# Kernel tuning notes

Measured on AMD Instinct MI355X. Metric: run time of the kernel, lower is better.

The kernel has to match this reference:

```python
import jax, jax.numpy as jnp
import numpy as np

DIM, HEADS, DIM_HEAD = 1024, 16, 64


def setup_inputs() -> dict:
    key = jax.random.key(0)
    k1, k2, k3, k4 = jax.random.split(key, 4)
    x = jax.random.normal(k1, (4, 2048, DIM), dtype=jnp.float32)
    # nn.Linear(dim, 3*dim, bias=False): weight [3*dim, dim]; y = x @ W.T
    W_qkv = jax.random.normal(k2, (3 * DIM, DIM), dtype=jnp.float32) * (DIM ** -0.5)
    W_proj = jax.random.normal(k3, (DIM, DIM), dtype=jnp.float32) * (DIM ** -0.5)
    b_proj = jax.random.normal(k4, (DIM,), dtype=jnp.float32) * 0.02
    return {"x": x, "W_qkv": W_qkv, "W_proj": W_proj, "b_proj": b_proj}


def reference(x, W_qkv, W_proj, b_proj):
    B, N, C = x.shape
    H, D = HEADS, DIM_HEAD
    scale = D ** -0.5
    qkv = x @ W_qkv.T                                   # [B, N, 3C]
    qkv = qkv.reshape(B, N, 3, H, D).transpose(2, 0, 3, 1, 4)  # [3, B, H, N, D]
    q, k, v = qkv[0], qkv[1], qkv[2]
    dots = jnp.einsum('bhid,bhjd->bhij', q, k) * scale  # [B, H, N, N]
    attn = jax.nn.softmax(dots, axis=-1)
    out = jnp.einsum('bhij,bhjd->bhid', attn, v)        # [B, H, N, D]
    out = out.transpose(0, 2, 1, 3).reshape(B, N, C)
    return out @ W_proj.T + b_proj
```

## Files before the change

### kernel.cpp

```cpp
#include <hip/hip_runtime.h>
#include <hip/hip_bf16.h>
#include <stdint.h>

typedef __bf16 bf16x4 __attribute__((ext_vector_type(4)));
typedef __bf16 bf16x8 __attribute__((ext_vector_type(8)));
typedef float  f32x4  __attribute__((ext_vector_type(4)));

#define LOG2E 1.44269504088896f

__device__ __forceinline__ bf16x8 cat8(bf16x4 a, bf16x4 b) {
    bf16x8 r;
    for (int i = 0; i < 4; ++i) { r[i] = a[i]; r[i + 4] = b[i]; }
    return r;
}

__device__ __forceinline__ void gl2lds16(const __bf16* g, __bf16* l) {
    __builtin_amdgcn_global_load_lds(
        (const __attribute__((address_space(1))) void*)g,
        (__attribute__((address_space(3))) void*)l, 16, 0, 0);
}

__global__ __launch_bounds__(256) void cvt_f32_bf16(const float* __restrict__ in,
                                                    __bf16* __restrict__ out) {
    size_t i = ((size_t)blockIdx.x * 256 + threadIdx.x) * 8;
    float4 a = ((const float4*)(in + i))[0];
    float4 b = ((const float4*)(in + i))[1];
    bf16x8 v;
    v[0] = (__bf16)a.x; v[1] = (__bf16)a.y; v[2] = (__bf16)a.z; v[3] = (__bf16)a.w;
    v[4] = (__bf16)b.x; v[5] = (__bf16)b.y; v[6] = (__bf16)b.z; v[7] = (__bf16)b.w;
    *(bf16x8*)(out + i) = v;
}

template<typename TC>
__global__ __launch_bounds__(256) void gemm_bt_bf16(
    const __bf16* __restrict__ A, const __bf16* __restrict__ B,
    const float* __restrict__ bias, TC* __restrict__ C,
    int M, int N, int K, int lda, int ldb, int ldc)
{
    __shared__ __bf16 As[128][32];
    __shared__ __bf16 Bs[128][32];
    const int tid = threadIdx.x;
    const int wave = tid >> 6, lane = tid & 63;
    const int lr = lane & 15, lq = lane >> 4;
    const int m0 = blockIdx.y * 128, n0 = blockIdx.x * 128;
    const int wm = (wave >> 1) * 64, wn = (wave & 1) * 64;

    f32x4 acc[4][4] = {};

    const int sr = lane >> 2;
    const int sc = (lane & 3) * 8;
    const __bf16* ag[2]; const __bf16* bg[2];
    __bf16* alds[2]; __bf16* blds[2];
    for (int t = 0; t < 2; ++t) {
        int chunk = wave * 2 + t;
        ag[t] = A + (size_t)(m0 + chunk * 16 + sr) * lda + sc;
        bg[t] = B + (size_t)(n0 + chunk * 16 + sr) * ldb + sc;
        alds[t] = &As[0][0] + chunk * 512;
        blds[t] = &Bs[0][0] + chunk * 512;
    }

    for (int k0 = 0; k0 < K; k0 += 32) {
        __syncthreads();
        gl2lds16(ag[0] + k0, alds[0]);
        gl2lds16(ag[1] + k0, alds[1]);
        gl2lds16(bg[0] + k0, blds[0]);
        gl2lds16(bg[1] + k0, blds[1]);
        __syncthreads();
        bf16x8 af[4], bf[4];
        for (int i = 0; i < 4; ++i) af[i] = *(const bf16x8*)&As[wm + i * 16 + lr][lq * 8];
        for (int j = 0; j < 4; ++j) bf[j] = *(const bf16x8*)&Bs[wn + j * 16 + lr][lq * 8];
        for (int i = 0; i < 4; ++i)
            for (int j = 0; j < 4; ++j)
                acc[i][j] = __builtin_amdgcn_mfma_f32_16x16x32_bf16(af[i], bf[j], acc[i][j], 0, 0, 0);
    }

    float bv[4] = {0.f, 0.f, 0.f, 0.f};
    if (bias)
        for (int j = 0; j < 4; ++j) bv[j] = bias[n0 + wn + j * 16 + lr];
    for (int i = 0; i < 4; ++i) {
        int row = m0 + wm + i * 16 + lq * 4;
        for (int j = 0; j < 4; ++j) {
            int col = n0 + wn + j * 16 + lr;
            for (int r = 0; r < 4; ++r) {
                float v = acc[i][j][r] + bv[j];
                C[(size_t)(row + r) * ldc + col] = (TC)v;
            }
        }
    }
}

__device__ __forceinline__ void stage16(const float* __restrict__ g, __bf16* l) {
    float4 a = ((const float4*)g)[0];
    float4 b = ((const float4*)g)[1];
    float4 c = ((const float4*)g)[2];
    float4 d = ((const float4*)g)[3];
    bf16x8 lo, hi;
    lo[0] = (__bf16)a.x; lo[1] = (__bf16)a.y; lo[2] = (__bf16)a.z; lo[3] = (__bf16)a.w;
    lo[4] = (__bf16)b.x; lo[5] = (__bf16)b.y; lo[6] = (__bf16)b.z; lo[7] = (__bf16)b.w;
    hi[0] = (__bf16)c.x; hi[1] = (__bf16)c.y; hi[2] = (__bf16)c.z; hi[3] = (__bf16)c.w;
    hi[4] = (__bf16)d.x; hi[5] = (__bf16)d.y; hi[6] = (__bf16)d.z; hi[7] = (__bf16)d.w;
    ((bf16x8*)l)[0] = lo;
    ((bf16x8*)l)[1] = hi;
}
__device__ __forceinline__ void stage16(const __bf16* __restrict__ g, __bf16* l) {
    ((bf16x8*)l)[0] = ((const bf16x8*)g)[0];
    ((bf16x8*)l)[1] = ((const bf16x8*)g)[1];
}

template<typename TA, typename TB, typename TC>
__global__ __launch_bounds__(256) void gemm_bt(
    const TA* __restrict__ A, const TB* __restrict__ B,
    const float* __restrict__ bias, TC* __restrict__ C,
    int M, int N, int K, int lda, int ldb, int ldc)
{
    __shared__ __bf16 As[128][40];
    __shared__ __bf16 Bs[128][40];
    const int tid = threadIdx.x;
    const int wave = tid >> 6, lane = tid & 63;
    const int lr = lane & 15, lq = lane >> 4;
    const int m0 = blockIdx.y * 128, n0 = blockIdx.x * 128;
    const int wm = (wave >> 1) * 64, wn = (wave & 1) * 64;
    const int srow = tid >> 1, scol = (tid & 1) * 16;

    f32x4 acc[4][4] = {};
    const TA* agp = A + (size_t)(m0 + srow) * lda + scol;
    const TB* bgp = B + (size_t)(n0 + srow) * ldb + scol;

    for (int k0 = 0; k0 < K; k0 += 32) {
        __syncthreads();
        stage16(agp + k0, &As[srow][scol]);
        stage16(bgp + k0, &Bs[srow][scol]);
        __syncthreads();
        bf16x8 af[4], bf[4];
        for (int i = 0; i < 4; ++i) af[i] = *(const bf16x8*)&As[wm + i * 16 + lr][lq * 8];
        for (int j = 0; j < 4; ++j) bf[j] = *(const bf16x8*)&Bs[wn + j * 16 + lr][lq * 8];
        for (int i = 0; i < 4; ++i)
            for (int j = 0; j < 4; ++j)
                acc[i][j] = __builtin_amdgcn_mfma_f32_16x16x32_bf16(af[i], bf[j], acc[i][j], 0, 0, 0);
    }

    float bv[4] = {0.f, 0.f, 0.f, 0.f};
    if (bias)
        for (int j = 0; j < 4; ++j) bv[j] = bias[n0 + wn + j * 16 + lr];
    for (int i = 0; i < 4; ++i) {
        int row = m0 + wm + i * 16 + lq * 4;
        for (int j = 0; j < 4; ++j) {
            int col = n0 + wn + j * 16 + lr;
            for (int r = 0; r < 4; ++r) {
                float v = acc[i][j][r] + bv[j];
                C[(size_t)(row + r) * ldc + col] = (TC)v;
            }
        }
    }
}

__global__ __launch_bounds__(256) void attn_kernel(__bf16* __restrict__ qkv)
{
    __shared__ __bf16 Ks[64][72];
    __shared__ __bf16 Vt[64][72];

    const int tid = threadIdx.x;
    const int wave = tid >> 6, lane = tid & 63;
    const int lr = lane & 15, lq = lane >> 4;

    const int bid = blockIdx.x;
    const int xcd = bid & 7, slot = bid >> 3;
    const int bh = xcd * 8 + (slot >> 4);
    const int qt = slot & 15;
    const int b = bh >> 4, h = bh & 15;
    const int rowbase = b * 2048;
    const int q0 = qt * 128;
    const float c1 = 0.125f * LOG2E;
    const float SHIFT = 8.0f;

    bf16x8 qf[2][2];
    for (int mt = 0; mt < 2; ++mt)
        for (int ks = 0; ks < 2; ++ks)
            qf[mt][ks] = *(const bf16x8*)(qkv +
                (size_t)(rowbase + q0 + wave * 32 + mt * 16 + lr) * 3072 + h * 64 + ks * 32 + lq * 8);

    float l_lane[2] = {0.f, 0.f};
    f32x4 o_acc[2][4] = {};

    const int kr = tid >> 2, kc = (tid & 3) * 16;
    const int vj0 = (tid & 15) * 4, vd0 = (tid >> 4) * 4;
    const __bf16* kbase = qkv + (size_t)(rowbase + kr) * 3072 + 1024 + h * 64 + kc;
    const __bf16* vbase = qkv + (size_t)(rowbase + vj0) * 3072 + 2048 + h * 64 + vd0;

    bf16x8 ka = ((const bf16x8*)kbase)[0];
    bf16x8 kb = ((const bf16x8*)kbase)[1];
    uint2 r0 = *(const uint2*)(vbase);
    uint2 r1 = *(const uint2*)(vbase + 3072);
    uint2 r2 = *(const uint2*)(vbase + 6144);
    uint2 r3 = *(const uint2*)(vbase + 9216);

    for (int it = 0; it < 32; ++it) {
        __syncthreads();
        *(bf16x8*)&Ks[kr][kc] = ka;
        *(bf16x8*)(&Ks[kr][kc] + 8) = kb;
        {
            uint2 c0 = { (r0.x & 0xffffu) | (r1.x << 16), (r2.x & 0xffffu) | (r3.x << 16) };
            uint2 c1v = { (r0.x >> 16) | (r1.x & 0xffff0000u), (r2.x >> 16) | (r3.x & 0xffff0000u) };
            uint2 c2 = { (r0.y & 0xffffu) | (r1.y << 16), (r2.y & 0xffffu) | (r3.y << 16) };
            uint2 c3 = { (r0.y >> 16) | (r1.y & 0xffff0000u), (r2.y >> 16) | (r3.y & 0xffff0000u) };
            *(uint2*)&Vt[vd0 + 0][vj0] = c0;
            *(uint2*)&Vt[vd0 + 1][vj0] = c1v;
            *(uint2*)&Vt[vd0 + 2][vj0] = c2;
            *(uint2*)&Vt[vd0 + 3][vj0] = c3;
        }
        __syncthreads();

        if (it + 1 < 32) {
            const __bf16* kg = kbase + (size_t)(it + 1) * 64 * 3072;
            ka = ((const bf16x8*)kg)[0];
            kb = ((const bf16x8*)kg)[1];
            const __bf16* vg = vbase + (size_t)(it + 1) * 64 * 3072;
            r0 = *(const uint2*)(vg);
            r1 = *(const uint2*)(vg + 3072);
            r2 = *(const uint2*)(vg + 6144);
            r3 = *(const uint2*)(vg + 9216);
        }

        f32x4 s[2][4] = {};
        for (int ks = 0; ks < 2; ++ks) {
            bf16x8 kf[4];
            for (int ntj = 0; ntj < 4; ++ntj)
                kf[ntj] = *(const bf16x8*)&Ks[ntj * 16 + lr][ks * 32 + lq * 8];
            for (int mt = 0; mt < 2; ++mt)
                for (int ntj = 0; ntj < 4; ++ntj)
                    s[mt][ntj] = __builtin_amdgcn_mfma_f32_16x16x32_bf16(kf[ntj], qf[mt][ks], s[mt][ntj], 0, 0, 0);
        }

        bf16x4 pf[2][4];
        for (int mt = 0; mt < 2; ++mt) {
            for (int ntj = 0; ntj < 4; ++ntj) {
                bf16x4 pk;
                for (int r = 0; r < 4; ++r) {
                    float p = __builtin_amdgcn_exp2f(s[mt][ntj][r] * c1 - SHIFT);
                    l_lane[mt] += p;
                    pk[r] = (__bf16)p;
                }
                pf[mt][ntj] = pk;
            }
        }

        for (int pi = 0; pi < 2; ++pi) {
            bf16x8 pfrag[2];
            for (int mt = 0; mt < 2; ++mt)
                pfrag[mt] = cat8(pf[mt][2 * pi], pf[mt][2 * pi + 1]);
            for (int dt = 0; dt < 4; ++dt) {
                bf16x4 vlo = *(const bf16x4*)&Vt[dt * 16 + lr][pi * 32 + lq * 4];
                bf16x4 vhi = *(const bf16x4*)&Vt[dt * 16 + lr][pi * 32 + 16 + lq * 4];
                bf16x8 vf = cat8(vlo, vhi);
                for (int mt = 0; mt < 2; ++mt)
                    o_acc[mt][dt] = __builtin_amdgcn_mfma_f32_16x16x32_bf16(vf, pfrag[mt], o_acc[mt][dt], 0, 0, 0);
            }
        }
    }

    for (int mt = 0; mt < 2; ++mt) {
        float l = l_lane[mt];
        l += __shfl_xor(l, 16);
        l += __shfl_xor(l, 32);
        float inv = 1.f / l;
        for (int dt = 0; dt < 4; ++dt) {
            bf16x4 ob;
            for (int r = 0; r < 4; ++r) ob[r] = (__bf16)(o_acc[mt][dt][r] * inv);
            *(bf16x4*)(qkv + (size_t)(rowbase + q0 + wave * 32 + mt * 16 + lr) * 3072 +
                       h * 64 + dt * 16 + lq * 4) = ob;
        }
    }
}

extern "C" void kernel_launch(void* const* d_in, const int* in_sizes, int n_in,
                              void* d_out, int out_size, void* d_ws, size_t ws_size,
                              hipStream_t stream) {
    const float* x     = (const float*)d_in[0];
    const float* Wqkv  = (const float*)d_in[1];
    const float* Wproj = (const float*)d_in[2];
    const float* bproj = (const float*)d_in[3];
    float* out   = (float*)d_out;
    __bf16* qkvb = (__bf16*)d_ws;

    const size_t QKV_E = (size_t)8192 * 3072;
    const size_t X_E   = (size_t)8192 * 1024;
    const size_t WQ_E  = (size_t)3072 * 1024;
    const size_t WP_E  = (size_t)1024 * 1024;
    const bool fast = ws_size >= (QKV_E + X_E + WQ_E + WP_E) * sizeof(__bf16);

    if (fast) {
        __bf16* xb  = qkvb + QKV_E;
        __bf16* wqb = xb + X_E;
        __bf16* wpb = wqb + WQ_E;
        cvt_f32_bf16<<<dim3((unsigned)(X_E / 2048)),  256, 0, stream>>>(x, xb);
        cvt_f32_bf16<<<dim3((unsigned)(WQ_E / 2048)), 256, 0, stream>>>(Wqkv, wqb);
        cvt_f32_bf16<<<dim3((unsigned)(WP_E / 2048)), 256, 0, stream>>>(Wproj, wpb);
        gemm_bt_bf16<__bf16><<<dim3(24, 64), 256, 0, stream>>>(
            xb, wqb, nullptr, qkvb, 8192, 3072, 1024, 1024, 1024, 3072);
        attn_kernel<<<dim3(1024), 256, 0, stream>>>(qkvb);
        gemm_bt_bf16<float><<<dim3(8, 64), 256, 0, stream>>>(
            qkvb, wpb, bproj, out, 8192, 1024, 1024, 3072, 1024, 1024);
    } else {
        gemm_bt<float, float, __bf16><<<dim3(24, 64), 256, 0, stream>>>(
            x, Wqkv, nullptr, qkvb, 8192, 3072, 1024, 1024, 1024, 3072);
        attn_kernel<<<dim3(1024), 256, 0, stream>>>(qkvb);
        gemm_bt<__bf16, float, float><<<dim3(8, 64), 256, 0, stream>>>(
            qkvb, Wproj, bproj, out, 8192, 1024, 1024, 3072, 1024, 1024);
    }
}
```

Baseline: 297.1 us.

## Double-buffer attention K/V tiles, permute V layout, add narrow projection GEMM

The attention kernel now keeps two LDS buffers for K and transposed V. The next tile is written after the current tile's compute, so each iteration needs only one barrier instead of two. V columns are stored in a permuted order so each MFMA operand comes from a single 16-byte LDS read instead of two 8-byte reads joined together. The output projection now uses a new 128x64-tile GEMM launched as 16x64 blocks, doubling the number of workgroups for the N=1024 problem so the GPU is better occupied. The cost is double the attention LDS and smaller per-block reuse in the projection GEMM.

```diff
diff --git a/kernel.cpp b/kernel.cpp
--- a/kernel.cpp
+++ b/kernel.cpp
@@ -85,6 +85,61 @@
                 float v = acc[i][j][r] + bv[j];
                 C[(size_t)(row + r) * ldc + col] = (TC)v;
             }
+        }
+    }
+}
+
+__global__ __launch_bounds__(256) void gemm_bt_bf16_n64(
+    const __bf16* __restrict__ A, const __bf16* __restrict__ B,
+    const float* __restrict__ bias, float* __restrict__ C,
+    int M, int N, int K, int lda, int ldb, int ldc)
+{
+    __shared__ __bf16 As[128][32];
+    __shared__ __bf16 Bs[64][32];
+    const int tid = threadIdx.x;
+    const int wave = tid >> 6, lane = tid & 63;
+    const int lr = lane & 15, lq = lane >> 4;
+    const int m0 = blockIdx.y * 128, n0 = blockIdx.x * 64;
+    const int wm = wave * 32;
+
+    f32x4 acc[2][4] = {};
+
+    const int sr = lane >> 2;
+    const int sc = (lane & 3) * 8;
+    const __bf16* gsrc[3]; __bf16* ldst[3];
+    for (int t = 0; t < 3; ++t) {
+        int c = wave * 3 + t;
+        if (c < 8) {
+            gsrc[t] = A + (size_t)(m0 + c * 16 + sr) * lda + sc;
+            ldst[t] = &As[0][0] + c * 512;
+        } else {
+            gsrc[t] = B + (size_t)(n0 + (c - 8) * 16 + sr) * ldb + sc;
+            ldst[t] = &Bs[0][0] + (c - 8) * 512;
+        }
+    }
+
+    for (int k0 = 0; k0 < K; k0 += 32) {
+        __syncthreads();
+        gl2lds16(gsrc[0] + k0, ldst[0]);
+        gl2lds16(gsrc[1] + k0, ldst[1]);
+        gl2lds16(gsrc[2] + k0, ldst[2]);
+        __syncthreads();
+        bf16x8 af[2], bf[4];
+        for (int i = 0; i < 2; ++i) af[i] = *(const bf16x8*)&As[wm + i * 16 + lr][lq * 8];
+        for (int j = 0; j < 4; ++j) bf[j] = *(const bf16x8*)&Bs[j * 16 + lr][lq * 8];
+        for (int i = 0; i < 2; ++i)
+            for (int j = 0; j < 4; ++j)
+                acc[i][j] = __builtin_amdgcn_mfma_f32_16x16x32_bf16(af[i], bf[j], acc[i][j], 0, 0, 0);
+    }
+
+    float bv[4];
+    for (int j = 0; j < 4; ++j) bv[j] = bias ? bias[n0 + j * 16 + lr] : 0.f;
+    for (int i = 0; i < 2; ++i) {
+        int row = m0 + wm + i * 16 + lq * 4;
+        for (int j = 0; j < 4; ++j) {
+            int col = n0 + j * 16 + lr;
+            for (int r = 0; r < 4; ++r)
+                C[(size_t)(row + r) * ldc + col] = acc[i][j][r] + bv[j];
         }
     }
 }
@@ -156,8 +211,8 @@
 
 __global__ __launch_bounds__(256) void attn_kernel(__bf16* __restrict__ qkv)
 {
-    __shared__ __bf16 Ks[64][72];
-    __shared__ __bf16 Vt[64][72];
+    __shared__ __bf16 Ks[2][64][72];
+    __shared__ __bf16 Vt[2][64][72];
 
     const int tid = threadIdx.x;
     const int wave = tid >> 6, lane = tid & 63;
@@ -183,31 +238,33 @@
     f32x4 o_acc[2][4] = {};
 
     const int kr = tid >> 2, kc = (tid & 3) * 16;
-    const int vj0 = (tid & 15) * 4, vd0 = (tid >> 4) * 4;
+    const int g0 = tid & 15;
+    const int vj0 = g0 * 4, vd0 = (tid >> 4) * 4;
+    const int vcol = ((g0 >> 3) * 32) + ((g0 & 3) * 8) + (((g0 >> 2) & 1) * 4);
     const __bf16* kbase = qkv + (size_t)(rowbase + kr) * 3072 + 1024 + h * 64 + kc;
     const __bf16* vbase = qkv + (size_t)(rowbase + vj0) * 3072 + 2048 + h * 64 + vd0;
 
     bf16x8 ka = ((const bf16x8*)kbase)[0];
     bf16x8 kb = ((const bf16x8*)kbase)[1];
-    uint2 r0 = *(const uint2*)(vbase);
-    uint2 r1 = *(const uint2*)(vbase + 3072);
-    uint2 r2 = *(const uint2*)(vbase + 6144);
-    uint2 r3 = *(const uint2*)(vbase + 9216);
+    uint2 t0 = *(const uint2*)(vbase);
+    uint2 t1 = *(const uint2*)(vbase + 3072);
+    uint2 t2 = *(const uint2*)(vbase + 6144);
+    uint2 t3 = *(const uint2*)(vbase + 9216);
+    {
+        *(bf16x8*)&Ks[0][kr][kc] = ka;
+        *(bf16x8*)(&Ks[0][kr][kc] + 8) = kb;
+        uint2 c0 = { (t0.x & 0xffffu) | (t1.x << 16), (t2.x & 0xffffu) | (t3.x << 16) };
+        uint2 d1 = { (t0.x >> 16) | (t1.x & 0xffff0000u), (t2.x >> 16) | (t3.x & 0xffff0000u) };
+        uint2 c2 = { (t0.y & 0xffffu) | (t1.y << 16), (t2.y & 0xffffu) | (t3.y << 16) };
+        uint2 d3 = { (t0.y >> 16) | (t1.y & 0xffff0000u), (t2.y >> 16) | (t3.y & 0xffff0000u) };
+        *(uint2*)&Vt[0][vd0 + 0][vcol] = c0;
+        *(uint2*)&Vt[0][vd0 + 1][vcol] = d1;
+        *(uint2*)&Vt[0][vd0 + 2][vcol] = c2;
+        *(uint2*)&Vt[0][vd0 + 3][vcol] = d3;
+    }
 
     for (int it = 0; it < 32; ++it) {
-        __syncthreads();
-        *(bf16x8*)&Ks[kr][kc] = ka;
-        *(bf16x8*)(&Ks[kr][kc] + 8) = kb;
-        {
-            uint2 c0 = { (r0.x & 0xffffu) | (r1.x << 16), (r2.x & 0xffffu) | (r3.x << 16) };
-            uint2 c1v = { (r0.x >> 16) | (r1.x & 0xffff0000u), (r2.x >> 16) | (r3.x & 0xffff0000u) };
-            uint2 c2 = { (r0.y & 0xffffu) | (r1.y << 16), (r2.y & 0xffffu) | (r3.y << 16) };
-            uint2 c3 = { (r0.y >> 16) | (r1.y & 0xffff0000u), (r2.y >> 16) | (r3.y & 0xffff0000u) };
-            *(uint2*)&Vt[vd0 + 0][vj0] = c0;
-            *(uint2*)&Vt[vd0 + 1][vj0] = c1v;
-            *(uint2*)&Vt[vd0 + 2][vj0] = c2;
-            *(uint2*)&Vt[vd0 + 3][vj0] = c3;
-        }
+        const int cur = it & 1;
         __syncthreads();
 
         if (it + 1 < 32) {
@@ -215,17 +272,17 @@
             ka = ((const bf16x8*)kg)[0];
             kb = ((const bf16x8*)kg)[1];
             const __bf16* vg = vbase + (size_t)(it + 1) * 64 * 3072;
-            r0 = *(const uint2*)(vg);
-            r1 = *(const uint2*)(vg + 3072);
-            r2 = *(const uint2*)(vg + 6144);
-            r3 = *(const uint2*)(vg + 9216);
+            t0 = *(const uint2*)(vg);
+            t1 = *(const uint2*)(vg + 3072);
+            t2 = *(const uint2*)(vg + 6144);
+            t3 = *(const uint2*)(vg + 9216);
         }
 
         f32x4 s[2][4] = {};
         for (int ks = 0; ks < 2; ++ks) {
             bf16x8 kf[4];
             for (int ntj = 0; ntj < 4; ++ntj)
-                kf[ntj] = *(const bf16x8*)&Ks[ntj * 16 + lr][ks * 32 + lq * 8];
+                kf[ntj] = *(const bf16x8*)&Ks[cur][ntj * 16 + lr][ks * 32 + lq * 8];
             for (int mt = 0; mt < 2; ++mt)
                 for (int ntj = 0; ntj < 4; ++ntj)
                     s[mt][ntj] = __builtin_amdgcn_mfma_f32_16x16x32_bf16(kf[ntj], qf[mt][ks], s[mt][ntj], 0, 0, 0);
@@ -249,12 +306,24 @@
             for (int mt = 0; mt < 2; ++mt)
                 pfrag[mt] = cat8(pf[mt][2 * pi], pf[mt][2 * pi + 1]);
             for (int dt = 0; dt < 4; ++dt) {
-                bf16x4 vlo = *(const bf16x4*)&Vt[dt * 16 + lr][pi * 32 + lq * 4];
-                bf16x4 vhi = *(const bf16x4*)&Vt[dt * 16 + lr][pi * 32 + 16 + lq * 4];
-                bf16x8 vf = cat8(vlo, vhi);
+                bf16x8 vf = *(const bf16x8*)&Vt[cur][dt * 16 + lr][pi * 32 + lq * 8];
                 for (int mt = 0; mt < 2; ++mt)
                     o_acc[mt][dt] = __builtin_amdgcn_mfma_f32_16x16x32_bf16(vf, pfrag[mt], o_acc[mt][dt], 0, 0, 0);
             }
+        }
+
+        if (it + 1 < 32) {
+            const int nb = cur ^ 1;
+            *(bf16x8*)&Ks[nb][kr][kc] = ka;
+            *(bf16x8*)(&Ks[nb][kr][kc] + 8) = kb;
+            uint2 c0 = { (t0.x & 0xffffu) | (t1.x << 16), (t2.x & 0xffffu) | (t3.x << 16) };
+            uint2 d1 = { (t0.x >> 16) | (t1.x & 0xffff0000u), (t2.x >> 16) | (t3.x & 0xffff0000u) };
+            uint2 c2 = { (t0.y & 0xffffu) | (t1.y << 16), (t2.y & 0xffffu) | (t3.y << 16) };
+            uint2 d3 = { (t0.y >> 16) | (t1.y & 0xffff0000u), (t2.y >> 16) | (t3.y & 0xffff0000u) };
+            *(uint2*)&Vt[nb][vd0 + 0][vcol] = c0;
+            *(uint2*)&Vt[nb][vd0 + 1][vcol] = d1;
+            *(uint2*)&Vt[nb][vd0 + 2][vcol] = c2;
+            *(uint2*)&Vt[nb][vd0 + 3][vcol] = d3;
         }
     }
 
@@ -298,7 +367,7 @@
         gemm_bt_bf16<__bf16><<<dim3(24, 64), 256, 0, stream>>>(
             xb, wqb, nullptr, qkvb, 8192, 3072, 1024, 1024, 1024, 3072);
         attn_kernel<<<dim3(1024), 256, 0, stream>>>(qkvb);
-        gemm_bt_bf16<float><<<dim3(8, 64), 256, 0, stream>>>(
+        gemm_bt_bf16_n64<<<dim3(16, 64), 256, 0, stream>>>(
             qkvb, wpb, bproj, out, 8192, 1024, 1024, 3072, 1024, 1024);
     } else {
         gemm_bt<float, float, __bf16><<<dim3(24, 64), 256, 0, stream>>>(
```

After: 304.0 us. +2.3%, slower.
